# Optimization experiments

Measured on AMD Instinct MI355X. Metric: run time of the kernel, lower is better.

The kernel has to match this reference:

```python
import jax, jax.numpy as jnp
import numpy as np

N, P, M, J, H = 32768, 5, 1024, 24, 256
SMPL_THRESH = 0.08


def _rand_transforms(rng, n):
    # random small-angle rotations + small translations -> invertible 4x4 joint transforms
    axis = rng.normal(size=(n, 3))
    axis /= np.linalg.norm(axis, axis=-1, keepdims=True)
    ang = rng.uniform(-0.5, 0.5, size=(n, 1, 1))
    K = np.zeros((n, 3, 3))
    K[:, 0, 1] = -axis[:, 2]; K[:, 0, 2] = axis[:, 1]
    K[:, 1, 0] = axis[:, 2];  K[:, 1, 2] = -axis[:, 0]
    K[:, 2, 0] = -axis[:, 1]; K[:, 2, 1] = axis[:, 0]
    R = np.eye(3)[None] + np.sin(ang) * K + (1.0 - np.cos(ang)) * (K @ K)
    T = np.zeros((n, 4, 4))
    T[:, :3, :3] = R
    T[:, :3, 3] = rng.normal(size=(n, 3)) * 0.1
    T[:, 3, 3] = 1.0
    return T.astype(np.float32)


def setup_inputs() -> dict:
    key = jax.random.key(0)
    ks = jax.random.split(key, 12)
    rng = np.random.default_rng(0)
    pose_pts = jax.random.normal(ks[0], (1, N, 3), jnp.float32) * 0.5
    pose_dirs = jax.random.normal(ks[1], (1, N, 3), jnp.float32)
    pose_dirs = pose_dirs / jnp.linalg.norm(pose_dirs, axis=-1, keepdims=True)
    part_pts = jax.random.normal(ks[2], (P, M, 3), jnp.float32) * 0.5
    part_pbw = jax.nn.softmax(jax.random.normal(ks[3], (P, M, J), jnp.float32), axis=-1)
    A = jnp.asarray(_rand_transforms(rng, J))[None]       # [1,24,4,4]
    big_A = jnp.asarray(_rand_transforms(rng, J))[None]   # [1,24,4,4]
    W1 = jax.random.normal(ks[4], (3, H), jnp.float32) * 0.1
    b1 = jnp.zeros((H,), jnp.float32)
    W2 = jax.random.normal(ks[5], (H, H), jnp.float32) * 0.06
    b2 = jnp.zeros((H,), jnp.float32)
    W3 = jax.random.normal(ks[6], (H, 3), jnp.float32) * 0.06
    b3 = jnp.zeros((3,), jnp.float32)
    lengths2 = jnp.full((P,), M, dtype=jnp.int32)
    return {"pose_pts": pose_pts, "pose_dirs": pose_dirs, "part_pts": part_pts,
            "part_pbw": part_pbw, "A": A, "big_A": big_A,
            "W1": W1, "b1": b1, "W2": W2, "b2": b2, "W3": W3, "b3": b3,
            "lengths2": lengths2}


def _lbs_pipeline(pose_pts, pose_dirs, part_pts, part_pbw, A, big_A,
                  W1, b1, W2, b2, W3, b3, lengths2):
    # ---- KNN (K=1) blend-weight lookup per part (torch.no_grad block) ----
    x = pose_pts[0]                                              # [N,3]
    d2 = (jnp.sum(x * x, -1)[:, None, None]
          - 2.0 * jnp.einsum('nd,pmd->npm', x, part_pts)
          + jnp.sum(part_pts * part_pts, -1)[None])              # [N,P,M]
    valid = jnp.arange(M)[None, :] < lengths2[:, None]           # [P,M]
    d2 = jnp.where(valid[None], jnp.maximum(d2, 0.0), jnp.inf)
    nn = jnp.argmin(d2, axis=-1)                                 # [N,P]
    pnorm = jnp.sqrt(jnp.take_along_axis(d2, nn[..., None], -1)[..., 0])  # [N,P]
    bw = part_pbw[jnp.arange(P)[None, :], nn]                    # [N,P,24]
    bw = jax.lax.stop_gradient(bw)
    pnorm = jax.lax.stop_gradient(pnorm)
    pflag = pnorm < SMPL_THRESH                                  # [N,P]

    # ---- gather-expand: each point assigned to every part ----
    pts_e = jnp.broadcast_to(x[:, None, :], (N, P, 3)).reshape(N * P, 3)
    dirs_e = jnp.broadcast_to(pose_dirs[0][:, None, :], (N, P, 3)).reshape(N * P, 3)
    bw_f = bw.reshape(N * P, J)

    # ---- per-point inverse linear blend skinning ----
    A_bw = jnp.einsum('kj,jxy->kxy', bw_f, A[0])                 # [NP,4,4]
    R_inv = jnp.linalg.inv(A_bw[:, :3, :3])
    tpts = jnp.einsum('kxy,ky->kx', R_inv, pts_e - A_bw[:, :3, 3])
    Ab = jnp.einsum('kj,jxy->kxy', bw_f, big_A[0])               # [NP,4,4]
    Rb = Ab[:, :3, :3]
    init_bigpose = jnp.einsum('kxy,ky->kx', Rb, tpts) + Ab[:, :3, 3]
    tdirs = jnp.einsum('kxy,ky->kx', R_inv, dirs_e)
    tpose_dirs = jnp.einsum('kxy,ky->kx', Rb, tdirs).reshape(1, N, P, 3)

    # ---- tpose deformer (residual MLP, masked by part flag) ----
    h = jax.nn.relu(init_bigpose @ W1 + b1)
    h = jax.nn.relu(h @ W2 + b2)
    resd = 0.05 * jnp.tanh(h @ W3 + b3)
    resd = resd * pflag.reshape(N * P, 1).astype(resd.dtype)
    tpose = (init_bigpose + resd).reshape(1, N, P, 3)
    return (tpose, tpose_dirs, resd.reshape(1, N, P, 3),
            pflag.reshape(1, N, P), init_bigpose[None], pnorm[None])


def reference(pose_pts, pose_dirs, part_pts, part_pbw, A, big_A,
              W1, b1, W2, b2, W3, b3, lengths2):
    return _lbs_pipeline(pose_pts, pose_dirs, part_pts, part_pbw, A, big_A,
                         W1, b1, W2, b2, W3, b3, lengths2)
```

## Files before the change

kernel.cpp:

```cpp
#include <hip/hip_runtime.h>
#include <stdint.h>
#include <math.h>

#define NPTS 32768
#define PP   5
#define MM   1024
#define JJ   24
#define HH   256

#define O0 0
#define O1 491520
#define O2 983040
#define O3 1474560
#define O4 1638400
#define O5 2129920

typedef unsigned short ushort_t;
typedef unsigned int   uint_t;
typedef unsigned long long u64_t;
typedef __attribute__((ext_vector_type(8))) short bf16x8;
typedef __attribute__((ext_vector_type(4))) float f32x4;
typedef __attribute__((ext_vector_type(2))) float f32x2;

__device__ __forceinline__ ushort_t f2bf(float f) {
  union { uint_t i; float f; } v; v.f = f;
  uint_t i = v.i;
  return (ushort_t)((i + 0x7FFFu + ((i >> 16) & 1u)) >> 16);
}
__device__ __forceinline__ uint_t cvt_pk_bf16(float lo, float hi) {
  uint_t r;
  asm("v_cvt_pk_bf16_f32 %0, %1, %2" : "=v"(r) : "v"(lo), "v"(hi));
  return r;
}
__device__ __forceinline__ float tanh_fast(float v) {
  v = fminf(fmaxf(v, -15.f), 15.f);
  float e = __expf(2.f*v);
  return __fdividef(e - 1.f, e + 1.f);
}

__device__ __forceinline__ void transform_one(
    int n, int p, int nn, float pn, float fl,
    float px, float py, float pz, float dx, float dy, float dz,
    const float* __restrict__ pbw,
    const float4* __restrict__ sA4, const float4* __restrict__ sB4,
    float* __restrict__ out)
{
  const float4* bwr = (const float4*)(pbw + ((size_t)p * MM + nn) * JJ);
  float bw[24];
  #pragma unroll
  for (int q = 0; q < 6; ++q) {
    float4 u = bwr[q];
    bw[q*4+0] = u.x; bw[q*4+1] = u.y; bw[q*4+2] = u.z; bw[q*4+3] = u.w;
  }

  float M1[12], M2[12];
  #pragma unroll
  for (int q = 0; q < 12; ++q) { M1[q] = 0.f; M2[q] = 0.f; }
  #pragma unroll
  for (int j = 0; j < 24; ++j) {
    float w = bw[j];
    float4 a0 = sA4[j*3+0], a1 = sA4[j*3+1], a2 = sA4[j*3+2];
    M1[0]=fmaf(w,a0.x,M1[0]); M1[1]=fmaf(w,a0.y,M1[1]); M1[2]=fmaf(w,a0.z,M1[2]); M1[3]=fmaf(w,a0.w,M1[3]);
    M1[4]=fmaf(w,a1.x,M1[4]); M1[5]=fmaf(w,a1.y,M1[5]); M1[6]=fmaf(w,a1.z,M1[6]); M1[7]=fmaf(w,a1.w,M1[7]);
    M1[8]=fmaf(w,a2.x,M1[8]); M1[9]=fmaf(w,a2.y,M1[9]); M1[10]=fmaf(w,a2.z,M1[10]); M1[11]=fmaf(w,a2.w,M1[11]);
    float4 c0 = sB4[j*3+0], c1 = sB4[j*3+1], c2 = sB4[j*3+2];
    M2[0]=fmaf(w,c0.x,M2[0]); M2[1]=fmaf(w,c0.y,M2[1]); M2[2]=fmaf(w,c0.z,M2[2]); M2[3]=fmaf(w,c0.w,M2[3]);
    M2[4]=fmaf(w,c1.x,M2[4]); M2[5]=fmaf(w,c1.y,M2[5]); M2[6]=fmaf(w,c1.z,M2[6]); M2[7]=fmaf(w,c1.w,M2[7]);
    M2[8]=fmaf(w,c2.x,M2[8]); M2[9]=fmaf(w,c2.y,M2[9]); M2[10]=fmaf(w,c2.z,M2[10]); M2[11]=fmaf(w,c2.w,M2[11]);
  }
  float a=M1[0], b=M1[1], c=M1[2];
  float d=M1[4], e=M1[5], f=M1[6];
  float g=M1[8], h=M1[9], i=M1[10];
  float C00 = e*i - f*h, C01 = c*h - b*i, C02 = b*f - c*e;
  float C10 = f*g - d*i, C11 = a*i - c*g, C12 = c*d - a*f;
  float C20 = d*h - e*g, C21 = b*g - a*h, C22 = a*e - b*d;
  float det = a*C00 + b*C10 + c*C20;
  float rd = 1.0f / det;
  float tx = px - M1[3], ty = py - M1[7], tz = pz - M1[11];
  float t0 = rd * (C00*tx + C01*ty + C02*tz);
  float t1 = rd * (C10*tx + C11*ty + C12*tz);
  float t2 = rd * (C20*tx + C21*ty + C22*tz);
  float i0 = M2[0]*t0 + M2[1]*t1 + M2[2]*t2  + M2[3];
  float i1 = M2[4]*t0 + M2[5]*t1 + M2[6]*t2  + M2[7];
  float i2 = M2[8]*t0 + M2[9]*t1 + M2[10]*t2 + M2[11];
  float d0 = rd * (C00*dx + C01*dy + C02*dz);
  float d1 = rd * (C10*dx + C11*dy + C12*dz);
  float d2 = rd * (C20*dx + C21*dy + C22*dz);
  float e0 = M2[0]*d0 + M2[1]*d1 + M2[2]*d2;
  float e1 = M2[4]*d0 + M2[5]*d1 + M2[6]*d2;
  float e2 = M2[8]*d0 + M2[9]*d1 + M2[10]*d2;

  size_t k = (size_t)n * PP + p;
  out[O1 + k*3+0] = e0; out[O1 + k*3+1] = e1; out[O1 + k*3+2] = e2;
  out[O3 + k] = fl;
  out[O4 + k*3+0] = i0; out[O4 + k*3+1] = i1; out[O4 + k*3+2] = i2;
  out[O5 + k] = pn;
}

__global__ __launch_bounds__(256) void nn_kernel(
    const float* __restrict__ pp0, const float* __restrict__ pp1,
    const float* __restrict__ part_pts, const float* __restrict__ pbw,
    const float* __restrict__ Ag, const float* __restrict__ Bg,
    const int* __restrict__ lengths2,
    const float* __restrict__ W2g, ushort_t* __restrict__ W2bf,
    float* __restrict__ out)
{
  if (blockIdx.x >= 1280) {
    int k = blockIdx.x - 1280;
    int n = threadIdx.x;
    float v = W2g[k*256 + n];
    int kc = k >> 5, quad = (k & 31) >> 3, j = k & 7;
    int tile = n >> 4, lane = quad*16 + (n & 15);
    W2bf[kc*8192 + tile*512 + lane*8 + j] = f2bf(v);
    return;
  }

  __shared__ float4 sXq[256], sYq[256], sZq[256], sWq[256];
  __shared__ float4 sA4[72];
  __shared__ float4 sB4[72];
  int t = threadIdx.x;
  int p  = blockIdx.x >> 8;
  int nb = blockIdx.x & 255;
  int g  = t >> 3;
  int s  = t & 7;
  int n0 = nb*128 + g*4;

  float s0r0 = pp0[0], s0r1 = pp0[1], s0r2 = pp0[2];
  float nrm = s0r0*s0r0 + s0r1*s0r1 + s0r2*s0r2;
  bool c0_is_dirs = fabsf(nrm - 1.0f) < 1e-4f;
  const float* pose_pts  = c0_is_dirs ? pp1 : pp0;
  const float* pose_dirs = c0_is_dirs ? pp0 : pp1;

  {
    #pragma clang fp contract(off)
    float* fX = (float*)sXq; float* fY = (float*)sYq;
    float* fZ = (float*)sZq; float* fW = (float*)sWq;
    for (int i = t; i < MM; i += 256) {
      float x = part_pts[((size_t)p*MM+i)*3+0];
      float y = part_pts[((size_t)p*MM+i)*3+1];
      float z = part_pts[((size_t)p*MM+i)*3+2];
      float yy = ((x*x) + (y*y)) + (z*z);
      fX[i] = x; fY[i] = y; fZ[i] = z; fW[i] = yy;
    }
  }
  for (int i = t; i < 72; i += 256) {
    int l = i*4;
    int j = l / 12, rc = l % 12;
    float4 qa, qb;
    qa.x = Ag[j*16+rc+0]; qa.y = Ag[j*16+rc+1]; qa.z = Ag[j*16+rc+2]; qa.w = Ag[j*16+rc+3];
    qb.x = Bg[j*16+rc+0]; qb.y = Bg[j*16+rc+1]; qb.z = Bg[j*16+rc+2]; qb.w = Bg[j*16+rc+3];
    sA4[i] = qa; sB4[i] = qb;
  }
  int mlen = lengths2[p]; if (mlen > MM) mlen = MM;
  __syncthreads();

  float X[4], Y[4], Z[4];
  f32x2 Xd[4], Yd[4], Zd[4], C2[4];
  {
    #pragma clang fp contract(off)
    const float4* pr = (const float4*)(pose_pts + (size_t)n0*3);
    float4 f0 = pr[0], f1 = pr[1], f2 = pr[2];
    X[0]=f0.x; Y[0]=f0.y; Z[0]=f0.z;
    X[1]=f0.w; Y[1]=f1.x; Z[1]=f1.y;
    X[2]=f1.z; Y[2]=f1.w; Z[2]=f2.x;
    X[3]=f2.y; Y[3]=f2.z; Z[3]=f2.w;
    #pragma unroll
    for (int j = 0; j < 4; ++j) {
      float x2 = ((X[j]*X[j]) + (Y[j]*Y[j])) + (Z[j]*Z[j]);
      Xd[j] = (f32x2){2.0f*X[j], 2.0f*X[j]};
      Yd[j] = (f32x2){2.0f*Y[j], 2.0f*Y[j]};
      Zd[j] = (f32x2){2.0f*Z[j], 2.0f*Z[j]};
      C2[j] = (f32x2){x2, x2};
    }
  }

  float best[4] = {INFINITY, INFINITY, INFINITY, INFINITY};
  int   code[4] = {0, 0, 0, 0};
  {
    #pragma clang fp contract(off)
    int nq = mlen >> 5;
    for (int k = 0; k < nq; ++k) {
      int qi = k*8 + s;
      float4 QX = sXq[qi], QY = sYq[qi], QZ = sZq[qi], QW = sWq[qi];
      f32x2 qx0 = {QX.x, QX.y}, qx1 = {QX.z, QX.w};
      f32x2 qy0 = {QY.x, QY.y}, qy1 = {QY.z, QY.w};
      f32x2 qz0 = {QZ.x, QZ.y}, qz1 = {QZ.z, QZ.w};
      f32x2 qw0 = {QW.x, QW.y}, qw1 = {QW.z, QW.w};
      int cb = k << 2;
      #pragma unroll
      for (int j = 0; j < 4; ++j) {
        f32x2 dt0 = ((Xd[j]*qx0) + (Yd[j]*qy0)) + (Zd[j]*qz0);
        f32x2 tt0 = (C2[j] - dt0) + qw0;
        f32x2 dt1 = ((Xd[j]*qx1) + (Yd[j]*qy1)) + (Zd[j]*qz1);
        f32x2 tt1 = (C2[j] - dt1) + qw1;
        float e0 = fmaxf(tt0.x, 0.f);
        float e1 = fmaxf(tt0.y, 0.f);
        float e2 = fmaxf(tt1.x, 0.f);
        float e3 = fmaxf(tt1.y, 0.f);
        bool l0 = e0 < best[j]; best[j] = fminf(best[j], e0); code[j] = l0 ? cb       : code[j];
        bool l1 = e1 < best[j]; best[j] = fminf(best[j], e1); code[j] = l1 ? (cb | 1) : code[j];
        bool l2 = e2 < best[j]; best[j] = fminf(best[j], e2); code[j] = l2 ? (cb | 2) : code[j];
        bool l3 = e3 < best[j]; best[j] = fminf(best[j], e3); code[j] = l3 ? (cb | 3) : code[j];
      }
    }
    int mb0 = nq << 5;
    if (mb0 < mlen) {
      const float* fX = (const float*)sXq; const float* fY = (const float*)sYq;
      const float* fZ = (const float*)sZq; const float* fW = (const float*)sWq;
      #pragma unroll
      for (int e = 0; e < 4; ++e) {
        int m = mb0 + 4*s + e;
        if (m < mlen) {
          float qx = fX[m], qy = fY[m], qz = fZ[m], qw = fW[m];
          int cc = (nq << 2) | e;
          #pragma unroll
          for (int j = 0; j < 4; ++j) {
            float dt2 = ((Xd[j].x*qx) + (Yd[j].x*qy)) + (Zd[j].x*qz);
            float dd = fmaxf((C2[j].x - dt2) + qw, 0.0f);
            bool lt = dd < best[j];
            best[j] = fminf(best[j], dd);
            code[j] = lt ? cc : code[j];
          }
        }
      }
    }
  }

  u64_t pk[4];
  #pragma unroll
  for (int j = 0; j < 4; ++j) {
    int mj = ((code[j] >> 2) << 5) + 4*s + (code[j] & 3);
    pk[j] = ((u64_t)__float_as_uint(best[j]) << 32) | (uint_t)mj;
    u64_t o;
    o = __shfl_xor(pk[j], 1); if (o < pk[j]) pk[j] = o;
    o = __shfl_xor(pk[j], 2); if (o < pk[j]) pk[j] = o;
    o = __shfl_xor(pk[j], 4); if (o < pk[j]) pk[j] = o;
  }

  if (s < 4) {
    u64_t mypk = (s==0) ? pk[0] : (s==1) ? pk[1] : (s==2) ? pk[2] : pk[3];
    float xa = (s==0) ? X[0] : (s==1) ? X[1] : (s==2) ? X[2] : X[3];
    float ya = (s==0) ? Y[0] : (s==1) ? Y[1] : (s==2) ? Y[2] : Y[3];
    float za = (s==0) ? Z[0] : (s==1) ? Z[1] : (s==2) ? Z[2] : Z[3];
    int n = n0 + s;
    int bm = (int)(mypk & 0xFFFFFFFFull);
    float bd = __uint_as_float((uint_t)(mypk >> 32));
    float pn = sqrtf(bd);
    float fl = ((double)pn < 0.08) ? 1.0f : 0.0f;
    float dxa = pose_dirs[n*3+0], dya = pose_dirs[n*3+1], dza = pose_dirs[n*3+2];
    transform_one(n, p, bm, pn, fl, xa, ya, za, dxa, dya, dza, pbw, sA4, sB4, out);
  }
}

__global__ __launch_bounds__(256) void mlp_kernel(
    const float* __restrict__ W1g, const float* __restrict__ b1g,
    const float* __restrict__ b2g, const float* __restrict__ W3g,
    const float* __restrict__ b3g, const ushort_t* __restrict__ W2bf,
    float* __restrict__ out)
{
  __shared__ struct {
    ushort_t B[2][8192];
    float4   w1c[256];
    float4   w3b2[256];
  } sm;

  int t = threadIdx.x;
  int wave = t >> 6, lane = t & 63, quad = lane >> 4, m16 = lane & 15;
  size_t row0 = (size_t)blockIdx.x * 64 + (size_t)wave * 16;

  auto stage = [&](int buf, int kc) {
    const ushort_t* src = W2bf + kc*8192 + wave*2048 + lane*8;
    #pragma unroll
    for (int i = 0; i < 4; ++i) {
      __builtin_amdgcn_global_load_lds(
        (const __attribute__((address_space(1))) void*)(src + i*512),
        (__attribute__((address_space(3))) void*)(&sm.B[buf][wave*2048 + i*512]),
        16, 0, 0);
    }
  };
  stage(0, 0);

  {
    int c = t;
    sm.w1c[c]  = make_float4(W1g[c], W1g[256+c], W1g[512+c], b1g[c]);
    sm.w3b2[c] = make_float4(W3g[c*3+0], W3g[c*3+1], W3g[c*3+2], b2g[c]);
  }

  int r0 = (int)row0 + m16;
  float x0 = out[O4 + (size_t)r0*3+0], y0 = out[O4 + (size_t)r0*3+1], z0 = out[O4 + (size_t)r0*3+2];

  f32x4 acc0[16];
  #pragma unroll
  for (int nt = 0; nt < 16; ++nt) acc0[nt] = (f32x4){0.f,0.f,0.f,0.f};

  int cur = 0;
  for (int kc = 0; kc < 8; ++kc) {
    asm volatile("s_waitcnt vmcnt(0)" ::: "memory");
    __syncthreads();
    if (kc < 7) stage(cur ^ 1, kc + 1);

    union { bf16x8 v; uint_t u[4]; } ua0;
    int c0 = kc*32 + quad*8;
    #pragma unroll
    for (int jj = 0; jj < 4; ++jj) {
      float4 wA = sm.w1c[c0 + 2*jj];
      float4 wB = sm.w1c[c0 + 2*jj + 1];
      float hA0 = fmaxf(fmaf(z0, wA.z, fmaf(y0, wA.y, fmaf(x0, wA.x, wA.w))), 0.f);
      float hB0 = fmaxf(fmaf(z0, wB.z, fmaf(y0, wB.y, fmaf(x0, wB.x, wB.w))), 0.f);
      ua0.u[jj] = cvt_pk_bf16(hA0, hB0);
    }

    const ushort_t* Bk = &sm.B[cur][lane*8];
    #pragma unroll
    for (int nt = 0; nt < 16; ++nt) {
      bf16x8 Bw = *(const bf16x8*)(Bk + nt*512);
      acc0[nt] = __builtin_amdgcn_mfma_f32_16x16x32_bf16(ua0.v, Bw, acc0[nt], 0, 0, 0);
    }
    cur ^= 1;
  }

  float flv = out[O3 + row0 + (size_t)m16];
  float ivx = out[O4 + (row0 + (size_t)m16)*3 + 0];
  float ivy = out[O4 + (row0 + (size_t)m16)*3 + 1];
  float ivz = out[O4 + (row0 + (size_t)m16)*3 + 2];

  float pr[4][3];
  #pragma unroll
  for (int reg = 0; reg < 4; ++reg) { pr[reg][0]=0.f; pr[reg][1]=0.f; pr[reg][2]=0.f; }
  #pragma unroll
  for (int nt = 0; nt < 16; ++nt) {
    float4 cv = sm.w3b2[nt*16 + m16];
    #pragma unroll
    for (int reg = 0; reg < 4; ++reg) {
      float h2 = fmaxf(acc0[nt][reg] + cv.w, 0.f);
      pr[reg][0] = fmaf(h2, cv.x, pr[reg][0]);
      pr[reg][1] = fmaf(h2, cv.y, pr[reg][1]);
      pr[reg][2] = fmaf(h2, cv.z, pr[reg][2]);
    }
  }
  float b30 = b3g[0], b31 = b3g[1], b32 = b3g[2];
  #pragma unroll
  for (int reg = 0; reg < 4; ++reg) {
    float p0 = pr[reg][0], p1 = pr[reg][1], p2 = pr[reg][2];
    #pragma unroll
    for (int mask = 1; mask < 16; mask <<= 1) {
      p0 += __shfl_xor(p0, mask);
      p1 += __shfl_xor(p1, mask);
      p2 += __shfl_xor(p2, mask);
    }
    int src = quad*4 + reg;
    float fl = __shfl(flv, src);
    float i0 = __shfl(ivx, src);
    float i1 = __shfl(ivy, src);
    float i2 = __shfl(ivz, src);
    if (m16 == 0) {
      int r = (int)row0 + src;
      float rr0 = 0.05f * tanh_fast(p0 + b30) * fl;
      float rr1 = 0.05f * tanh_fast(p1 + b31) * fl;
      float rr2 = 0.05f * tanh_fast(p2 + b32) * fl;
      out[O0 + (size_t)r*3+0] = i0 + rr0;
      out[O0 + (size_t)r*3+1] = i1 + rr1;
      out[O0 + (size_t)r*3+2] = i2 + rr2;
      out[O2 + (size_t)r*3+0] = rr0;
      out[O2 + (size_t)r*3+1] = rr1;
      out[O2 + (size_t)r*3+2] = rr2;
    }
  }
}

extern "C" void kernel_launch(void* const* d_in, const int* in_sizes, int n_in,
                              void* d_out, int out_size, void* d_ws, size_t ws_size,
                              hipStream_t stream) {
  (void)out_size; (void)ws_size;
  const int want[13] = {98304, 98304, 15360, 122880, 384, 384, 768, 256, 65536, 256, 768, 3, 5};
  int idx[13];
  bool used[64] = {false};
  for (int L = 0; L < 13; ++L) {
    idx[L] = -1;
    for (int s = 0; s < n_in && s < 64; ++s) {
      if (!used[s] && in_sizes[s] == want[L]) { idx[L] = s; used[s] = true; break; }
    }
    if (idx[L] < 0) idx[L] = L;
  }
  const float* pp0       = (const float*)d_in[idx[0]];
  const float* pp1       = (const float*)d_in[idx[1]];
  const float* part_pts  = (const float*)d_in[idx[2]];
  const float* part_pbw  = (const float*)d_in[idx[3]];
  const float* A         = (const float*)d_in[idx[4]];
  const float* bigA      = (const float*)d_in[idx[5]];
  const float* W1        = (const float*)d_in[idx[6]];
  const float* b1        = (const float*)d_in[idx[7]];
  const float* W2        = (const float*)d_in[idx[8]];
  const float* b2        = (const float*)d_in[idx[9]];
  const float* W3        = (const float*)d_in[idx[10]];
  const float* b3        = (const float*)d_in[idx[11]];
  const int*   lengths2  = (const int*)d_in[idx[12]];
  float* out = (float*)d_out;
  ushort_t* W2bf = (ushort_t*)d_ws;

  nn_kernel<<<1536, 256, 0, stream>>>(pp0, pp1, part_pts, part_pbw,
                                      A, bigA, lengths2, W2, W2bf, out);
  mlp_kernel<<<2560, 256, 0, stream>>>(W1, b1, b2, W3, b3, W2bf, out);
}
```

Baseline: 176.8 us.

## Load W2 bf16 fragments directly from global into registers instead of LDS

Drops the double-buffered LDS staging of W2 (global_load_lds plus a per-chunk barrier). Each lane now reads its bf16 W2 fragments straight from global memory, relying on L2/L1 since every block reads the same weights. Register double-buffering in groups of four tiles overlaps those loads with the MFMAs. This removes eight barriers and cuts LDS use, which may raise occupancy. The cost is more global/L1 traffic per wave and higher register pressure.

After: 183.7 us. 1.04x slower.

```diff
diff --git a/kernel.cpp b/kernel.cpp
--- a/kernel.cpp
+++ b/kernel.cpp
@@ -258,65 +258,59 @@
     const float* __restrict__ b3g, const ushort_t* __restrict__ W2bf,
     float* __restrict__ out)
 {
-  __shared__ struct {
-    ushort_t B[2][8192];
-    float4   w1c[256];
-    float4   w3b2[256];
-  } sm;
+  __shared__ float4 w1c[256];
+  __shared__ float4 w3b2[256];
 
   int t = threadIdx.x;
   int wave = t >> 6, lane = t & 63, quad = lane >> 4, m16 = lane & 15;
   size_t row0 = (size_t)blockIdx.x * 64 + (size_t)wave * 16;
 
-  auto stage = [&](int buf, int kc) {
-    const ushort_t* src = W2bf + kc*8192 + wave*2048 + lane*8;
-    #pragma unroll
-    for (int i = 0; i < 4; ++i) {
-      __builtin_amdgcn_global_load_lds(
-        (const __attribute__((address_space(1))) void*)(src + i*512),
-        (__attribute__((address_space(3))) void*)(&sm.B[buf][wave*2048 + i*512]),
-        16, 0, 0);
-    }
-  };
-  stage(0, 0);
-
   {
     int c = t;
-    sm.w1c[c]  = make_float4(W1g[c], W1g[256+c], W1g[512+c], b1g[c]);
-    sm.w3b2[c] = make_float4(W3g[c*3+0], W3g[c*3+1], W3g[c*3+2], b2g[c]);
+    w1c[c]  = make_float4(W1g[c], W1g[256+c], W1g[512+c], b1g[c]);
+    w3b2[c] = make_float4(W3g[c*3+0], W3g[c*3+1], W3g[c*3+2], b2g[c]);
   }
 
   int r0 = (int)row0 + m16;
   float x0 = out[O4 + (size_t)r0*3+0], y0 = out[O4 + (size_t)r0*3+1], z0 = out[O4 + (size_t)r0*3+2];
+  __syncthreads();
 
   f32x4 acc0[16];
   #pragma unroll
   for (int nt = 0; nt < 16; ++nt) acc0[nt] = (f32x4){0.f,0.f,0.f,0.f};
 
-  int cur = 0;
+  const ushort_t* Wlane = W2bf + lane*8;
+  #pragma unroll 1
   for (int kc = 0; kc < 8; ++kc) {
-    asm volatile("s_waitcnt vmcnt(0)" ::: "memory");
-    __syncthreads();
-    if (kc < 7) stage(cur ^ 1, kc + 1);
+    const ushort_t* Bk = Wlane + kc*8192;
+    bf16x8 Bcur[4], Bnxt[4];
+    #pragma unroll
+    for (int q = 0; q < 4; ++q) Bcur[q] = *(const bf16x8*)(Bk + q*512);
 
     union { bf16x8 v; uint_t u[4]; } ua0;
     int c0 = kc*32 + quad*8;
     #pragma unroll
     for (int jj = 0; jj < 4; ++jj) {
-      float4 wA = sm.w1c[c0 + 2*jj];
-      float4 wB = sm.w1c[c0 + 2*jj + 1];
+      float4 wA = w1c[c0 + 2*jj];
+      float4 wB = w1c[c0 + 2*jj + 1];
       float hA0 = fmaxf(fmaf(z0, wA.z, fmaf(y0, wA.y, fmaf(x0, wA.x, wA.w))), 0.f);
       float hB0 = fmaxf(fmaf(z0, wB.z, fmaf(y0, wB.y, fmaf(x0, wB.x, wB.w))), 0.f);
       ua0.u[jj] = cvt_pk_bf16(hA0, hB0);
     }
 
-    const ushort_t* Bk = &sm.B[cur][lane*8];
-    #pragma unroll
-    for (int nt = 0; nt < 16; ++nt) {
-      bf16x8 Bw = *(const bf16x8*)(Bk + nt*512);
-      acc0[nt] = __builtin_amdgcn_mfma_f32_16x16x32_bf16(ua0.v, Bw, acc0[nt], 0, 0, 0);
-    }
-    cur ^= 1;
+    #pragma unroll
+    for (int gq = 0; gq < 4; ++gq) {
+      if (gq < 3) {
+        #pragma unroll
+        for (int q = 0; q < 4; ++q)
+          Bnxt[q] = *(const bf16x8*)(Bk + (gq+1)*2048 + q*512);
+      }
+      #pragma unroll
+      for (int q = 0; q < 4; ++q)
+        acc0[gq*4+q] = __builtin_amdgcn_mfma_f32_16x16x32_bf16(ua0.v, Bcur[q], acc0[gq*4+q], 0, 0, 0);
+      #pragma unroll
+      for (int q = 0; q < 4; ++q) Bcur[q] = Bnxt[q];
+    }
   }
 
   float flv = out[O3 + row0 + (size_t)m16];
@@ -329,7 +323,7 @@
   for (int reg = 0; reg < 4; ++reg) { pr[reg][0]=0.f; pr[reg][1]=0.f; pr[reg][2]=0.f; }
   #pragma unroll
   for (int nt = 0; nt < 16; ++nt) {
-    float4 cv = sm.w3b2[nt*16 + m16];
+    float4 cv = w3b2[nt*16 + m16];
     #pragma unroll
     for (int reg = 0; reg < 4; ++reg) {
       float h2 = fmaxf(acc0[nt][reg] + cv.w, 0.f);
```
